# Kernel tuning notes

Hardware: AMD Instinct MI355X
Metric: run time of the kernel (lower is better)

The kernel has to match this reference:

```python
import jax, jax.numpy as jnp
import numpy as np

B, S, D, K = 16, 4096, 256, 1024


def setup_inputs() -> dict:
    key = jax.random.key(0)
    k1, k2 = jax.random.split(key)
    z_e = jax.random.normal(k1, (B, S, D), dtype=jnp.float32)
    # nn.Embedding weight initialized uniform(-1/K, 1/K)
    codebook = jax.random.uniform(k2, (K, D), dtype=jnp.float32,
                                  minval=-1.0 / K, maxval=1.0 / K)
    return {"z_e": z_e, "codebook": codebook}


def reference(z_e, codebook):
    # straight_through path of VQEmbedding
    d = codebook.shape[1]
    x = z_e.reshape(-1, d)                                   # [N, D]
    dist = (jnp.sum(x * x, axis=1, keepdims=True)
            + jnp.sum(codebook * codebook, axis=1)
            - 2.0 * (x @ codebook.T))                        # [N, K]
    idx = jnp.argmin(dist, axis=1)                           # [N]
    codes = jnp.take(codebook, idx, axis=0).reshape(z_e.shape)  # gather
    z_q = z_e + jax.lax.stop_gradient(codes - z_e)           # straight-through codes (detached codebook)
    z_q_bar = codes                                          # codes with grad to codebook
    return (z_q, z_q_bar)
```

## Files before the change

### kernel.cpp

```cpp
#include <hip/hip_runtime.h>
#include <stdint.h>

#define D 256
#define KCODES 1024
#define NROWS 65536

using int4v  = __attribute__((ext_vector_type(4))) int;
using f32x4v = __attribute__((ext_vector_type(4))) float;

__device__ __forceinline__ float rne_f(float x) { return __builtin_rintf(x); }

__device__ __forceinline__ void gl_lds16(const void* g, void* l) {
  __builtin_amdgcn_global_load_lds(
      (const __attribute__((address_space(1))) void*)g,
      (__attribute__((address_space(3))) void*)l, 16, 0, 0);
}

__device__ __forceinline__ void dig4(float t, int* d) {
  float f0 = rne_f(t);  float t1 = __fmul_rn(__fsub_rn(t, f0), 256.0f);
  float f1 = rne_f(t1); float t2 = __fmul_rn(__fsub_rn(t1, f1), 256.0f);
  float f2 = rne_f(t2); float t3 = __fmul_rn(__fsub_rn(t2, f2), 256.0f);
  float f3 = rne_f(t3);
  int d0 = (int)f0, d1 = (int)f1, d2 = (int)f2, d3 = (int)f3;
  if (d3 == 128) { d3 = -128; ++d2; }
  if (d2 == 128) { d2 = -128; ++d1; }
  if (d1 == 128) { d1 = -128; ++d0; }
  d[0] = d0; d[1] = d1; d[2] = d2; d[3] = d3;
}

__device__ __forceinline__ float np_block128_sumsq(const float* __restrict__ q) {
  float r[8], v[8];
  *(float4*)(v) = *(const float4*)(q);
  *(float4*)(v + 4) = *(const float4*)(q + 4);
#pragma unroll
  for (int j = 0; j < 8; ++j) r[j] = __fmul_rn(v[j], v[j]);
  for (int i = 8; i < 128; i += 8) {
    *(float4*)(v) = *(const float4*)(q + i);
    *(float4*)(v + 4) = *(const float4*)(q + i + 4);
#pragma unroll
    for (int j = 0; j < 8; ++j) r[j] = __fadd_rn(r[j], __fmul_rn(v[j], v[j]));
  }
  float t01 = __fadd_rn(r[0], r[1]);
  float t23 = __fadd_rn(r[2], r[3]);
  float t45 = __fadd_rn(r[4], r[5]);
  float t67 = __fadd_rn(r[6], r[7]);
  return __fadd_rn(__fadd_rn(t01, t23), __fadd_rn(t45, t67));
}
__device__ __forceinline__ float np_sumsq256(const float* __restrict__ q) {
  return __fadd_rn(np_block128_sumsq(q), np_block128_sumsq(q + 128));
}

__global__ __launch_bounds__(256) void prep_all(const float* __restrict__ z,
                                                const float* __restrict__ cb,
                                                float* __restrict__ c2,
                                                float* __restrict__ srow,
                                                char* __restrict__ cbd) {
  __shared__ float zs[64][260];
  const int bid = blockIdx.x;
  const int tid = threadIdx.x;
  if (bid < 1040) {
    const float* src; float* dst; int r0;
    if (bid < 1024) { r0 = bid * 64; src = z; dst = srow; }
    else            { r0 = (bid - 1024) * 64; src = cb; dst = c2; }
#pragma unroll
    for (int it = 0; it < 16; ++it) {
      int g = tid + it * 256, row = g >> 6, f4 = g & 63;
      *(float4*)(&zs[row][f4 * 4]) = *(const float4*)(src + (size_t)(r0 + row) * D + f4 * 4);
    }
    __syncthreads();
    if (tid < 64) dst[r0 + tid] = np_sumsq256(&zs[tid][0]);
    return;
  }
  int id = (bid - 1040) * 256 + tid;
  int n = id >> 4, kc = id & 15;
  int f = kc >> 2, kg = kc & 3, nt = n >> 5, c = n & 31;
  const float* src = cb + (size_t)n * D + kc * 16;
  float v[16];
  *(float4*)(v) = *(const float4*)(src);
  *(float4*)(v + 4) = *(const float4*)(src + 4);
  *(float4*)(v + 8) = *(const float4*)(src + 8);
  *(float4*)(v + 12) = *(const float4*)(src + 12);
  int dg[16][4];
#pragma unroll
  for (int e = 0; e < 16; ++e) dig4(v[e] * 65536.0f, dg[e]);
  size_t base = (size_t)nt * 8192 + f * 2048 + (c >> 4) * 1024 + kg * 256 + (c & 15) * 16;
#pragma unroll
  for (int p = 0; p < 4; ++p) {
    int4v wv;
#pragma unroll
    for (int wi = 0; wi < 4; ++wi)
      wv[wi] = (dg[wi * 4][p] & 255) | ((dg[wi * 4 + 1][p] & 255) << 8) |
               ((dg[wi * 4 + 2][p] & 255) << 16) | (dg[wi * 4 + 3][p] << 24);
    *(int4v*)(cbd + (size_t)p * (KCODES * 256) + base) = wv;
  }
}

#define BM 64
#define BN 16
#define NT (KCODES / BN)

#define MFI16(a, b, c) __builtin_amdgcn_mfma_i32_16x16x64_i8((a), (b), (c), 0, 0, 0)

__global__ __launch_bounds__(256, 4) void vq_mfma(
    const float* __restrict__ z, const float* __restrict__ cb,
    const float* __restrict__ c2g, const float* __restrict__ srowg,
    const char* __restrict__ cbd, float* __restrict__ out) {
  __shared__ alignas(16) char bbuf[2][16384];
  __shared__ float c2s[KCODES];
  __shared__ int bidx_s[BM];

  const int tid = threadIdx.x;
  const int lane = tid & 63;
  const int w = tid >> 6;
  const int r0 = blockIdx.x * BM;
  const int l15 = lane & 15, l4 = lane >> 4;

  c2s[tid] = c2g[tid];
  c2s[tid + 256] = c2g[tid + 256];
  c2s[tid + 512] = c2g[tid + 512];
  c2s[tid + 768] = c2g[tid + 768];

  float sr[4];
#pragma unroll
  for (int r = 0; r < 4; ++r) sr[r] = srowg[r0 + w * 16 + l4 * 4 + r];

  int4v Adig[4][4];
  {
    const float* zr = z + (size_t)(r0 + w * 16 + l15) * D + l4 * 16;
#pragma unroll
    for (int f = 0; f < 4; ++f) {
      float v[16];
      *(float4*)(v) = *(const float4*)(zr + f * 64);
      *(float4*)(v + 4) = *(const float4*)(zr + f * 64 + 4);
      *(float4*)(v + 8) = *(const float4*)(zr + f * 64 + 8);
      *(float4*)(v + 12) = *(const float4*)(zr + f * 64 + 12);
      int dg[16][4];
#pragma unroll
      for (int e = 0; e < 16; ++e) dig4(v[e] * 16.0f, dg[e]);
#pragma unroll
      for (int p = 0; p < 4; ++p) {
        int4v wv;
#pragma unroll
        for (int wi = 0; wi < 4; ++wi)
          wv[wi] = (dg[wi * 4][p] & 255) | ((dg[wi * 4 + 1][p] & 255) << 8) |
                   ((dg[wi * 4 + 2][p] & 255) << 16) | (dg[wi * 4 + 3][p] << 24);
        Adig[p][f] = wv;
      }
    }
  }

  const char* cbd_b = cbd;
#define STAGE(ntv, dstbase) do { \
    const char* s_ = cbd_b + (size_t)((ntv) >> 1) * 8192 + (tid >> 6) * 2048 + \
                     ((ntv) & 1) * 1024 + (tid & 63) * 16; \
    char* d_ = (dstbase) + (tid >> 6) * 1024 + (tid & 63) * 16; \
    gl_lds16(s_,          d_); \
    gl_lds16(s_ + 262144, d_ + 4096); \
    gl_lds16(s_ + 524288, d_ + 8192); \
    gl_lds16(s_ + 786432, d_ + 12288); \
  } while (0)

#define LOADB(set, basep, kf) do { \
    const char* pk_ = (basep) + (kf) * 1024; \
    B0##set = *(const int4v*)(pk_); \
    B1##set = *(const int4v*)(pk_ + 4096); \
    B2##set = *(const int4v*)(pk_ + 8192); \
    B3##set = *(const int4v*)(pk_ + 12288); \
  } while (0)

#define CLUSTER(set, kf) do { \
    acc[1] = MFI16(Adig[0][kf], B1##set, acc[1]); \
    acc[3] = MFI16(Adig[0][kf], B3##set, acc[3]); \
    acc[2] = MFI16(Adig[0][kf], B2##set, acc[2]); \
    acc[1] = MFI16(Adig[1][kf], B0##set, acc[1]); \
    acc[3] = MFI16(Adig[1][kf], B2##set, acc[3]); \
    acc[2] = MFI16(Adig[1][kf], B1##set, acc[2]); \
    acc[0] = MFI16(Adig[0][kf], B0##set, acc[0]); \
    acc[3] = MFI16(Adig[2][kf], B1##set, acc[3]); \
    acc[2] = MFI16(Adig[2][kf], B0##set, acc[2]); \
    acc[3] = MFI16(Adig[3][kf], B0##set, acc[3]); \
  } while (0)

#define CLUSTER0(set) do { \
    acc[1] = MFI16(Adig[0][0], B1##set, ZZ); \
    acc[3] = MFI16(Adig[0][0], B3##set, ZZ); \
    acc[2] = MFI16(Adig[0][0], B2##set, ZZ); \
    acc[1] = MFI16(Adig[1][0], B0##set, acc[1]); \
    acc[3] = MFI16(Adig[1][0], B2##set, acc[3]); \
    acc[2] = MFI16(Adig[1][0], B1##set, acc[2]); \
    acc[0] = MFI16(Adig[0][0], B0##set, ZZ); \
    acc[3] = MFI16(Adig[2][0], B1##set, acc[3]); \
    acc[2] = MFI16(Adig[2][0], B0##set, acc[2]); \
    acc[3] = MFI16(Adig[3][0], B0##set, acc[3]); \
  } while (0)

  float bd[4]; int bi[4];
#pragma unroll
  for (int r = 0; r < 4; ++r) { bd[r] = 3.4e38f; bi[r] = 0x7fffffff; }

  const int4v ZZ = {0, 0, 0, 0};
  int4v acc[4];
  int4v B0a, B1a, B2a, B3a;
  int4v B0b, B1b, B2b, B3b;

  STAGE(0, &bbuf[0][0]);
  __syncthreads();

  for (int nt = 0; nt < NT; ++nt) {
    const char* basep = &bbuf[nt & 1][0] + lane * 16;
    if (nt + 1 < NT) STAGE(nt + 1, &bbuf[(nt + 1) & 1][0]);

    LOADB(a, basep, 0);
    LOADB(b, basep, 1);
    CLUSTER0(a);
    LOADB(a, basep, 2);
    CLUSTER(b, 1);
    LOADB(b, basep, 3);
    CLUSTER(a, 2);
    CLUSTER(b, 3);

    {
      const int kc = nt * BN + l15;
      const float c2v = c2s[kc];
#pragma unroll
      for (int r = 0; r < 4; ++r) {
        int hi32 = acc[0][r] * 256 + acc[1][r];
        double lo_d = fma((double)acc[2][r], 256.0, (double)acc[3][r]);
        double md = fma((double)hi32, 65536.0, lo_d) * 0x1p-44;
        float mf = (float)md;
        float dist = __fsub_rn(__fadd_rn(sr[r], c2v), __fmul_rn(2.0f, mf));
        if (dist < bd[r]) { bd[r] = dist; bi[r] = kc; }
      }
    }
    __syncthreads();
  }

#pragma unroll
  for (int r = 0; r < 4; ++r) {
#pragma unroll
    for (int m = 1; m < 16; m <<= 1) {
      float od = __shfl_xor(bd[r], m);
      int oi = __shfl_xor(bi[r], m);
      if (od < bd[r] || (od == bd[r] && oi < bi[r])) { bd[r] = od; bi[r] = oi; }
    }
    if (l15 == 0) bidx_s[w * 16 + l4 * 4 + r] = bi[r];
  }
  __syncthreads();

  {
    float* out0 = out;
    float* out1 = out + (size_t)NROWS * D;
#pragma unroll
    for (int rr = 0; rr < 16; ++rr) {
      const int row_l = w * 16 + rr;
      const int grow = r0 + row_l;
      const int kb = bidx_s[row_l];
      f32x4v c4 = *(const f32x4v*)(cb + (size_t)kb * D + lane * 4);
      f32x4v z4 = *(const f32x4v*)(z + (size_t)grow * D + lane * 4);
      f32x4v q;
      q.x = __fadd_rn(z4.x, __fsub_rn(c4.x, z4.x));
      q.y = __fadd_rn(z4.y, __fsub_rn(c4.y, z4.y));
      q.z = __fadd_rn(z4.z, __fsub_rn(c4.z, z4.z));
      q.w = __fadd_rn(z4.w, __fsub_rn(c4.w, z4.w));
      __builtin_nontemporal_store(q, (f32x4v*)(out0 + (size_t)grow * D + lane * 4));
      __builtin_nontemporal_store(c4, (f32x4v*)(out1 + (size_t)grow * D + lane * 4));
    }
  }
}

__global__ void c2_kernel_fb(const float* __restrict__ cb, float* __restrict__ c2) {
  int k = blockIdx.x * blockDim.x + threadIdx.x;
  if (k < KCODES) c2[k] = np_sumsq256(cb + (size_t)k * D);
}

__global__ __launch_bounds__(256) void vq_fallback(const float* __restrict__ z,
                                                   const float* __restrict__ cb,
                                                   const float* __restrict__ c2,
                                                   float* __restrict__ out) {
  __shared__ float zs[64][260];
  __shared__ float cs[64][260];
  __shared__ float srow[64];
  __shared__ int bidx[64];
  const int tid = threadIdx.x;
  const int tx = tid & 15, ty = tid >> 4;
  const int r0 = blockIdx.x * 64;
#pragma unroll
  for (int it = 0; it < 16; ++it) {
    int g = tid + it * 256, row = g >> 6, f4 = g & 63;
    *(float4*)(&zs[row][f4 * 4]) = *(const float4*)(z + (size_t)(r0 + row) * D + f4 * 4);
  }
  __syncthreads();
  if (tid < 64) srow[tid] = np_sumsq256(&zs[tid][0]);
  float bd[4]; int bi[4];
#pragma unroll
  for (int j = 0; j < 4; ++j) { bd[j] = 3.4e38f; bi[j] = 0x7fffffff; }
  for (int t = 0; t < KCODES / 64; ++t) {
    __syncthreads();
#pragma unroll
    for (int it = 0; it < 16; ++it) {
      int g = tid + it * 256, row = g >> 6, f4 = g & 63;
      *(float4*)(&cs[row][f4 * 4]) = *(const float4*)(cb + (size_t)(t * 64 + row) * D + f4 * 4);
    }
    __syncthreads();
    double acc[4][4];
#pragma unroll
    for (int j = 0; j < 4; ++j)
#pragma unroll
      for (int i = 0; i < 4; ++i) acc[j][i] = 0.0;
#pragma unroll 2
    for (int d = 0; d < D; d += 4) {
      float4 a[4], b[4];
#pragma unroll
      for (int j = 0; j < 4; ++j) a[j] = *(const float4*)(&zs[ty + 16 * j][d]);
#pragma unroll
      for (int i = 0; i < 4; ++i) b[i] = *(const float4*)(&cs[tx + 16 * i][d]);
#pragma unroll
      for (int j = 0; j < 4; ++j)
#pragma unroll
        for (int i = 0; i < 4; ++i) {
          acc[j][i] += (double)a[j].x * (double)b[i].x;
          acc[j][i] += (double)a[j].y * (double)b[i].y;
          acc[j][i] += (double)a[j].z * (double)b[i].z;
          acc[j][i] += (double)a[j].w * (double)b[i].w;
        }
    }
#pragma unroll
    for (int j = 0; j < 4; ++j) {
      const float s = srow[ty + 16 * j];
#pragma unroll
      for (int i = 0; i < 4; ++i) {
        const int k = t * 64 + tx + 16 * i;
        const float m = (float)acc[j][i];
        const float dist = __fsub_rn(__fadd_rn(s, c2[k]), __fmul_rn(2.0f, m));
        if (dist < bd[j]) { bd[j] = dist; bi[j] = k; }
      }
    }
  }
  __syncthreads();
  float* red_d = &cs[0][0];
  int* red_i = (int*)&cs[20][0];
#pragma unroll
  for (int j = 0; j < 4; ++j) {
    red_d[(ty + 16 * j) * 16 + tx] = bd[j];
    red_i[(ty + 16 * j) * 16 + tx] = bi[j];
  }
  __syncthreads();
  if (tid < 64) {
    float best = red_d[tid * 16 + 0];
    int bsti = red_i[tid * 16 + 0];
    for (int x = 1; x < 16; ++x) {
      float d2 = red_d[tid * 16 + x]; int i2 = red_i[tid * 16 + x];
      if (d2 < best || (d2 == best && i2 < bsti)) { best = d2; bsti = i2; }
    }
    bidx[tid] = bsti;
  }
  __syncthreads();
  const int wid = tid >> 6, lane = tid & 63;
  float* out0 = out;
  float* out1 = out + (size_t)NROWS * D;
  for (int r = wid; r < 64; r += 4) {
    const int gr = r0 + r;
    const int kb = bidx[r];
    float4 c4 = *(const float4*)(cb + (size_t)kb * D + lane * 4);
    float4 z4 = *(const float4*)(&zs[r][lane * 4]);
    float4 q;
    q.x = __fadd_rn(z4.x, __fsub_rn(c4.x, z4.x));
    q.y = __fadd_rn(z4.y, __fsub_rn(c4.y, z4.y));
    q.z = __fadd_rn(z4.z, __fsub_rn(c4.z, z4.z));
    q.w = __fadd_rn(z4.w, __fsub_rn(c4.w, z4.w));
    *(float4*)(out0 + (size_t)gr * D + lane * 4) = q;
    *(float4*)(out1 + (size_t)gr * D + lane * 4) = c4;
  }
}

extern "C" void kernel_launch(void* const* d_in, const int* in_sizes, int n_in,
                              void* d_out, int out_size, void* d_ws, size_t ws_size,
                              hipStream_t stream) {
  const float* z = (const float*)d_in[0];
  const float* cb = (const float*)d_in[1];
  float* out = (float*)d_out;

  const size_t c2_off = 0;
  const size_t srow_off = 4096;
  const size_t cbd_off = 4096 + 262144;
  const size_t need = cbd_off + (size_t)4 * KCODES * 256;

  if (ws_size < need) {
    float* c2 = (float*)d_ws;
    c2_kernel_fb<<<KCODES / 256, 256, 0, stream>>>(cb, c2);
    vq_fallback<<<NROWS / 64, 256, 0, stream>>>(z, cb, c2, out);
    return;
  }

  float* c2 = (float*)((char*)d_ws + c2_off);
  float* srow = (float*)((char*)d_ws + srow_off);
  char* cbd = (char*)d_ws + cbd_off;

  prep_all<<<1104, 256, 0, stream>>>(z, cb, c2, srow, cbd);
  vq_mfma<<<NROWS / BM, 256, 0, stream>>>(z, cb, c2, srow, cbd, out);
}
```

Measured before the change: 172.7 us.

## Rotate per-wave k-fragment order and prefetch next tile's first B fragment

Each wave now walks the four k-fragments in a rotated order (starting at w&3), so different waves read different LDS regions at the same time. The first B fragment of the next codebook tile is loaded from LDS before the loop-end barrier, after a vmcnt(0) wait, so that LDS read latency overlaps the last MFMA cluster. The factor of 2 in the distance is folded into the fixed-point scale constant, removing one multiply. The early read relies only on the calling thread's own vmcnt wait, not on a block-wide barrier, so it may read LDS data still being written by other waves' global_load_lds.

```diff
diff --git a/kernel.cpp b/kernel.cpp
--- a/kernel.cpp
+++ b/kernel.cpp
@@ -125,15 +125,17 @@
   for (int r = 0; r < 4; ++r) sr[r] = srowg[r0 + w * 16 + l4 * 4 + r];
 
   int4v Adig[4][4];
+  const int kfr[4] = {w & 3, (w + 1) & 3, (w + 2) & 3, (w + 3) & 3};
   {
-    const float* zr = z + (size_t)(r0 + w * 16 + l15) * D + l4 * 16;
-#pragma unroll
-    for (int f = 0; f < 4; ++f) {
+    const float* zrow = z + (size_t)(r0 + w * 16 + l15) * D + l4 * 16;
+#pragma unroll
+    for (int i = 0; i < 4; ++i) {
+      const float* zr = zrow + kfr[i] * 64;
       float v[16];
-      *(float4*)(v) = *(const float4*)(zr + f * 64);
-      *(float4*)(v + 4) = *(const float4*)(zr + f * 64 + 4);
-      *(float4*)(v + 8) = *(const float4*)(zr + f * 64 + 8);
-      *(float4*)(v + 12) = *(const float4*)(zr + f * 64 + 12);
+      *(float4*)(v) = *(const float4*)(zr);
+      *(float4*)(v + 4) = *(const float4*)(zr + 4);
+      *(float4*)(v + 8) = *(const float4*)(zr + 8);
+      *(float4*)(v + 12) = *(const float4*)(zr + 12);
       int dg[16][4];
 #pragma unroll
       for (int e = 0; e < 16; ++e) dig4(v[e] * 16.0f, dg[e]);
@@ -144,7 +146,7 @@
         for (int wi = 0; wi < 4; ++wi)
           wv[wi] = (dg[wi * 4][p] & 255) | ((dg[wi * 4 + 1][p] & 255) << 8) |
                    ((dg[wi * 4 + 2][p] & 255) << 16) | (dg[wi * 4 + 3][p] << 24);
-        Adig[p][f] = wv;
+        Adig[p][i] = wv;
       }
     }
   }
@@ -160,25 +162,25 @@
     gl_lds16(s_ + 786432, d_ + 12288); \
   } while (0)
 
-#define LOADB(set, basep, kf) do { \
-    const char* pk_ = (basep) + (kf) * 1024; \
+#define LOADB(set, basep, kfv) do { \
+    const char* pk_ = (basep) + (kfv) * 1024; \
     B0##set = *(const int4v*)(pk_); \
     B1##set = *(const int4v*)(pk_ + 4096); \
     B2##set = *(const int4v*)(pk_ + 8192); \
     B3##set = *(const int4v*)(pk_ + 12288); \
   } while (0)
 
-#define CLUSTER(set, kf) do { \
-    acc[1] = MFI16(Adig[0][kf], B1##set, acc[1]); \
-    acc[3] = MFI16(Adig[0][kf], B3##set, acc[3]); \
-    acc[2] = MFI16(Adig[0][kf], B2##set, acc[2]); \
-    acc[1] = MFI16(Adig[1][kf], B0##set, acc[1]); \
-    acc[3] = MFI16(Adig[1][kf], B2##set, acc[3]); \
-    acc[2] = MFI16(Adig[1][kf], B1##set, acc[2]); \
-    acc[0] = MFI16(Adig[0][kf], B0##set, acc[0]); \
-    acc[3] = MFI16(Adig[2][kf], B1##set, acc[3]); \
-    acc[2] = MFI16(Adig[2][kf], B0##set, acc[2]); \
-    acc[3] = MFI16(Adig[3][kf], B0##set, acc[3]); \
+#define CLUSTER(set, ai) do { \
+    acc[1] = MFI16(Adig[0][ai], B1##set, acc[1]); \
+    acc[3] = MFI16(Adig[0][ai], B3##set, acc[3]); \
+    acc[2] = MFI16(Adig[0][ai], B2##set, acc[2]); \
+    acc[1] = MFI16(Adig[1][ai], B0##set, acc[1]); \
+    acc[3] = MFI16(Adig[1][ai], B2##set, acc[3]); \
+    acc[2] = MFI16(Adig[1][ai], B1##set, acc[2]); \
+    acc[0] = MFI16(Adig[0][ai], B0##set, acc[0]); \
+    acc[3] = MFI16(Adig[2][ai], B1##set, acc[3]); \
+    acc[2] = MFI16(Adig[2][ai], B0##set, acc[2]); \
+    acc[3] = MFI16(Adig[3][ai], B0##set, acc[3]); \
   } while (0)
 
 #define CLUSTER0(set) do { \
@@ -205,18 +207,23 @@
 
   STAGE(0, &bbuf[0][0]);
   __syncthreads();
+  { const char* bp0 = &bbuf[0][0] + lane * 16; LOADB(a, bp0, kfr[0]); }
 
   for (int nt = 0; nt < NT; ++nt) {
     const char* basep = &bbuf[nt & 1][0] + lane * 16;
     if (nt + 1 < NT) STAGE(nt + 1, &bbuf[(nt + 1) & 1][0]);
 
-    LOADB(a, basep, 0);
-    LOADB(b, basep, 1);
+    LOADB(b, basep, kfr[1]);
     CLUSTER0(a);
-    LOADB(a, basep, 2);
+    LOADB(a, basep, kfr[2]);
     CLUSTER(b, 1);
-    LOADB(b, basep, 3);
+    LOADB(b, basep, kfr[3]);
     CLUSTER(a, 2);
+    if (nt + 1 < NT) {
+      asm volatile("s_waitcnt vmcnt(0)" ::: "memory");
+      const char* nbase = &bbuf[(nt + 1) & 1][0] + lane * 16;
+      LOADB(a, nbase, kfr[0]);
+    }
     CLUSTER(b, 3);
 
     {
@@ -226,9 +233,8 @@
       for (int r = 0; r < 4; ++r) {
         int hi32 = acc[0][r] * 256 + acc[1][r];
         double lo_d = fma((double)acc[2][r], 256.0, (double)acc[3][r]);
-        double md = fma((double)hi32, 65536.0, lo_d) * 0x1p-44;
-        float mf = (float)md;
-        float dist = __fsub_rn(__fadd_rn(sr[r], c2v), __fmul_rn(2.0f, mf));
+        float mf2 = (float)(fma((double)hi32, 65536.0, lo_d) * 0x1p-43);
+        float dist = __fsub_rn(__fadd_rn(sr[r], c2v), mf2);
         if (dist < bd[r]) { bd[r] = dist; bi[r] = kc; }
       }
     }
```

After: 173.8 us. About the same (+0.7%).

## Double rows per wave so each staged codebook tile feeds two MFMA row groups

Applied to the files above, without the earlier changes.

Each wave now handles 32 rows instead of 16, keeping two sets of int8 digit A fragments and accumulators, so every codebook tile loaded from LDS is reused across twice as many rows. The block tile grows to 128 rows, which halves the block count and the total codebook staging traffic per row. Occupancy bounds drop from 4 to 2 blocks per CU to make room for the extra registers. The doubling of the dot product is folded into the final scale factor. The cost is heavier register pressure and fewer resident waves to hide latency.

```diff
diff --git a/kernel.cpp b/kernel.cpp
--- a/kernel.cpp
+++ b/kernel.cpp
@@ -95,13 +95,13 @@
   }
 }
 
-#define BM 64
+#define BM 128
 #define BN 16
 #define NT (KCODES / BN)
 
 #define MFI16(a, b, c) __builtin_amdgcn_mfma_i32_16x16x64_i8((a), (b), (c), 0, 0, 0)
 
-__global__ __launch_bounds__(256, 4) void vq_mfma(
+__global__ __launch_bounds__(256, 2) void vq_mfma(
     const float* __restrict__ z, const float* __restrict__ cb,
     const float* __restrict__ c2g, const float* __restrict__ srowg,
     const char* __restrict__ cbd, float* __restrict__ out) {
@@ -120,20 +120,24 @@
   c2s[tid + 512] = c2g[tid + 512];
   c2s[tid + 768] = c2g[tid + 768];
 
-  float sr[4];
-#pragma unroll
-  for (int r = 0; r < 4; ++r) sr[r] = srowg[r0 + w * 16 + l4 * 4 + r];
-
-  int4v Adig[4][4];
-  {
-    const float* zr = z + (size_t)(r0 + w * 16 + l15) * D + l4 * 16;
+  float sr[8];
+#pragma unroll
+  for (int fi = 0; fi < 2; ++fi)
+#pragma unroll
+    for (int r = 0; r < 4; ++r)
+      sr[fi * 4 + r] = srowg[r0 + w * 32 + fi * 16 + l4 * 4 + r];
+
+  int4v AdA[4][4], AdB[4][4];
+#pragma unroll
+  for (int fi = 0; fi < 2; ++fi) {
+    const float* zr0 = z + (size_t)(r0 + w * 32 + fi * 16 + l15) * D + l4 * 16;
 #pragma unroll
     for (int f = 0; f < 4; ++f) {
       float v[16];
-      *(float4*)(v) = *(const float4*)(zr + f * 64);
-      *(float4*)(v + 4) = *(const float4*)(zr + f * 64 + 4);
-      *(float4*)(v + 8) = *(const float4*)(zr + f * 64 + 8);
-      *(float4*)(v + 12) = *(const float4*)(zr + f * 64 + 12);
+      *(float4*)(v) = *(const float4*)(zr0 + f * 64);
+      *(float4*)(v + 4) = *(const float4*)(zr0 + f * 64 + 4);
+      *(float4*)(v + 8) = *(const float4*)(zr0 + f * 64 + 8);
+      *(float4*)(v + 12) = *(const float4*)(zr0 + f * 64 + 12);
       int dg[16][4];
 #pragma unroll
       for (int e = 0; e < 16; ++e) dig4(v[e] * 16.0f, dg[e]);
@@ -144,7 +148,7 @@
         for (int wi = 0; wi < 4; ++wi)
           wv[wi] = (dg[wi * 4][p] & 255) | ((dg[wi * 4 + 1][p] & 255) << 8) |
                    ((dg[wi * 4 + 2][p] & 255) << 16) | (dg[wi * 4 + 3][p] << 24);
-        Adig[p][f] = wv;
+        if (fi == 0) AdA[p][f] = wv; else AdB[p][f] = wv;
       }
     }
   }
@@ -168,38 +172,58 @@
     B3##set = *(const int4v*)(pk_ + 12288); \
   } while (0)
 
-#define CLUSTER(set, kf) do { \
-    acc[1] = MFI16(Adig[0][kf], B1##set, acc[1]); \
-    acc[3] = MFI16(Adig[0][kf], B3##set, acc[3]); \
-    acc[2] = MFI16(Adig[0][kf], B2##set, acc[2]); \
-    acc[1] = MFI16(Adig[1][kf], B0##set, acc[1]); \
-    acc[3] = MFI16(Adig[1][kf], B2##set, acc[3]); \
-    acc[2] = MFI16(Adig[1][kf], B1##set, acc[2]); \
-    acc[0] = MFI16(Adig[0][kf], B0##set, acc[0]); \
-    acc[3] = MFI16(Adig[2][kf], B1##set, acc[3]); \
-    acc[2] = MFI16(Adig[2][kf], B0##set, acc[2]); \
-    acc[3] = MFI16(Adig[3][kf], B0##set, acc[3]); \
+#define CLUSTER2(set, kf) do { \
+    accA[1] = MFI16(AdA[0][kf], B1##set, accA[1]); \
+    accB[1] = MFI16(AdB[0][kf], B1##set, accB[1]); \
+    accA[3] = MFI16(AdA[0][kf], B3##set, accA[3]); \
+    accB[3] = MFI16(AdB[0][kf], B3##set, accB[3]); \
+    accA[2] = MFI16(AdA[0][kf], B2##set, accA[2]); \
+    accB[2] = MFI16(AdB[0][kf], B2##set, accB[2]); \
+    accA[1] = MFI16(AdA[1][kf], B0##set, accA[1]); \
+    accB[1] = MFI16(AdB[1][kf], B0##set, accB[1]); \
+    accA[3] = MFI16(AdA[1][kf], B2##set, accA[3]); \
+    accB[3] = MFI16(AdB[1][kf], B2##set, accB[3]); \
+    accA[2] = MFI16(AdA[1][kf], B1##set, accA[2]); \
+    accB[2] = MFI16(AdB[1][kf], B1##set, accB[2]); \
+    accA[0] = MFI16(AdA[0][kf], B0##set, accA[0]); \
+    accB[0] = MFI16(AdB[0][kf], B0##set, accB[0]); \
+    accA[3] = MFI16(AdA[2][kf], B1##set, accA[3]); \
+    accB[3] = MFI16(AdB[2][kf], B1##set, accB[3]); \
+    accA[2] = MFI16(AdA[2][kf], B0##set, accA[2]); \
+    accB[2] = MFI16(AdB[2][kf], B0##set, accB[2]); \
+    accA[3] = MFI16(AdA[3][kf], B0##set, accA[3]); \
+    accB[3] = MFI16(AdB[3][kf], B0##set, accB[3]); \
   } while (0)
 
-#define CLUSTER0(set) do { \
-    acc[1] = MFI16(Adig[0][0], B1##set, ZZ); \
-    acc[3] = MFI16(Adig[0][0], B3##set, ZZ); \
-    acc[2] = MFI16(Adig[0][0], B2##set, ZZ); \
-    acc[1] = MFI16(Adig[1][0], B0##set, acc[1]); \
-    acc[3] = MFI16(Adig[1][0], B2##set, acc[3]); \
-    acc[2] = MFI16(Adig[1][0], B1##set, acc[2]); \
-    acc[0] = MFI16(Adig[0][0], B0##set, ZZ); \
-    acc[3] = MFI16(Adig[2][0], B1##set, acc[3]); \
-    acc[2] = MFI16(Adig[2][0], B0##set, acc[2]); \
-    acc[3] = MFI16(Adig[3][0], B0##set, acc[3]); \
+#define CLUSTER20(set) do { \
+    accA[1] = MFI16(AdA[0][0], B1##set, ZZ); \
+    accB[1] = MFI16(AdB[0][0], B1##set, ZZ); \
+    accA[3] = MFI16(AdA[0][0], B3##set, ZZ); \
+    accB[3] = MFI16(AdB[0][0], B3##set, ZZ); \
+    accA[2] = MFI16(AdA[0][0], B2##set, ZZ); \
+    accB[2] = MFI16(AdB[0][0], B2##set, ZZ); \
+    accA[1] = MFI16(AdA[1][0], B0##set, accA[1]); \
+    accB[1] = MFI16(AdB[1][0], B0##set, accB[1]); \
+    accA[3] = MFI16(AdA[1][0], B2##set, accA[3]); \
+    accB[3] = MFI16(AdB[1][0], B2##set, accB[3]); \
+    accA[2] = MFI16(AdA[1][0], B1##set, accA[2]); \
+    accB[2] = MFI16(AdB[1][0], B1##set, accB[2]); \
+    accA[0] = MFI16(AdA[0][0], B0##set, ZZ); \
+    accB[0] = MFI16(AdB[0][0], B0##set, ZZ); \
+    accA[3] = MFI16(AdA[2][0], B1##set, accA[3]); \
+    accB[3] = MFI16(AdB[2][0], B1##set, accB[3]); \
+    accA[2] = MFI16(AdA[2][0], B0##set, accA[2]); \
+    accB[2] = MFI16(AdB[2][0], B0##set, accB[2]); \
+    accA[3] = MFI16(AdA[3][0], B0##set, accA[3]); \
+    accB[3] = MFI16(AdB[3][0], B0##set, accB[3]); \
   } while (0)
 
-  float bd[4]; int bi[4];
-#pragma unroll
-  for (int r = 0; r < 4; ++r) { bd[r] = 3.4e38f; bi[r] = 0x7fffffff; }
+  float bd[8]; int bi[8];
+#pragma unroll
+  for (int r = 0; r < 8; ++r) { bd[r] = 3.4e38f; bi[r] = 0x7fffffff; }
 
   const int4v ZZ = {0, 0, 0, 0};
-  int4v acc[4];
+  int4v accA[4], accB[4];
   int4v B0a, B1a, B2a, B3a;
   int4v B0b, B1b, B2b, B3b;
 
@@ -212,38 +236,45 @@
 
     LOADB(a, basep, 0);
     LOADB(b, basep, 1);
-    CLUSTER0(a);
+    CLUSTER20(a);
     LOADB(a, basep, 2);
-    CLUSTER(b, 1);
+    CLUSTER2(b, 1);
     LOADB(b, basep, 3);
-    CLUSTER(a, 2);
-    CLUSTER(b, 3);
+    CLUSTER2(a, 2);
+    CLUSTER2(b, 3);
 
     {
       const int kc = nt * BN + l15;
       const float c2v = c2s[kc];
 #pragma unroll
       for (int r = 0; r < 4; ++r) {
-        int hi32 = acc[0][r] * 256 + acc[1][r];
-        double lo_d = fma((double)acc[2][r], 256.0, (double)acc[3][r]);
-        double md = fma((double)hi32, 65536.0, lo_d) * 0x1p-44;
-        float mf = (float)md;
-        float dist = __fsub_rn(__fadd_rn(sr[r], c2v), __fmul_rn(2.0f, mf));
+        int hi32 = accA[0][r] * 256 + accA[1][r];
+        double lo_d = fma((double)accA[2][r], 256.0, (double)accA[3][r]);
+        float mf2 = (float)(fma((double)hi32, 65536.0, lo_d) * 0x1p-43);
+        float dist = __fsub_rn(__fadd_rn(sr[r], c2v), mf2);
         if (dist < bd[r]) { bd[r] = dist; bi[r] = kc; }
       }
+#pragma unroll
+      for (int r = 0; r < 4; ++r) {
+        int hi32 = accB[0][r] * 256 + accB[1][r];
+        double lo_d = fma((double)accB[2][r], 256.0, (double)accB[3][r]);
+        float mf2 = (float)(fma((double)hi32, 65536.0, lo_d) * 0x1p-43);
+        float dist = __fsub_rn(__fadd_rn(sr[4 + r], c2v), mf2);
+        if (dist < bd[4 + r]) { bd[4 + r] = dist; bi[4 + r] = kc; }
+      }
     }
     __syncthreads();
   }
 
 #pragma unroll
-  for (int r = 0; r < 4; ++r) {
+  for (int r = 0; r < 8; ++r) {
 #pragma unroll
     for (int m = 1; m < 16; m <<= 1) {
       float od = __shfl_xor(bd[r], m);
       int oi = __shfl_xor(bi[r], m);
       if (od < bd[r] || (od == bd[r] && oi < bi[r])) { bd[r] = od; bi[r] = oi; }
     }
-    if (l15 == 0) bidx_s[w * 16 + l4 * 4 + r] = bi[r];
+    if (l15 == 0) bidx_s[w * 32 + (r >> 2) * 16 + l4 * 4 + (r & 3)] = bi[r];
   }
   __syncthreads();
 
@@ -251,8 +282,8 @@
     float* out0 = out;
     float* out1 = out + (size_t)NROWS * D;
 #pragma unroll
-    for (int rr = 0; rr < 16; ++rr) {
-      const int row_l = w * 16 + rr;
+    for (int rr = 0; rr < 32; ++rr) {
+      const int row_l = w * 32 + rr;
       const int grow = r0 + row_l;
       const int kb = bidx_s[row_l];
       f32x4v c4 = *(const f32x4v*)(cb + (size_t)kb * D + lane * 4);
```

New measurement: 167.5 us (median of 2 runs). 3.0% less time.
